# Kernel optimization log

Measured on AMD Instinct MI355X. Metric: run time of the kernel, lower is better.

## Reference

```python
import jax, jax.numpy as jnp
import numpy as np
from jax import lax

PH = PW = 7  # patch size


def _unfold2d(x, ph, pw):
    # x: [B, C, H, W] -> patches [B*Ho*Wo, C*ph*pw], channel-major like F.unfold
    B, C, H, W = x.shape
    patches = lax.conv_general_dilated_patches(
        x, filter_shape=(ph, pw), window_strides=(1, 1), padding='VALID')
    # patches: [B, C*ph*pw, Ho, Wo] with feature order (c, i, j) matching F.unfold
    Ho, Wo = H - ph + 1, W - pw + 1
    D = C * ph * pw
    q2d = patches.reshape(B, D, Ho * Wo).transpose(0, 2, 1).reshape(B * Ho * Wo, D)
    return q2d, (B, C, H, W, Ho, Wo, D)


def _fold2d_mean(res, shape_info):
    # res: [B*Ho*Wo, D] patch values -> overlap-add mean image [B, C, H, W]
    B, C, H, W, Ho, Wo, D = shape_info
    res = res.reshape(B, Ho, Wo, C, PH, PW)
    out = jnp.zeros((B, C, H, W), dtype=res.dtype)
    cnt = jnp.zeros((H, W), dtype=res.dtype)
    for di in range(PH):          # small fixed 7x7 loop over patch offsets
        for dj in range(PW):
            out = out.at[:, :, di:di + Ho, dj:dj + Wo].add(
                res[:, :, :, :, di, dj].transpose(0, 3, 1, 2))
            cnt = cnt.at[di:di + Ho, dj:dj + Wo].add(1.0)
    return out / cnt  # reduce='mean'


def setup_inputs() -> dict:
    key = jax.random.key(0)
    k1, k2, k3 = jax.random.split(key, 3)
    query = jax.random.normal(k1, (1, 3, 96, 96), dtype=jnp.float32)
    kmat = jax.random.normal(k2, (8100, 147), dtype=jnp.float32)
    vmat = jax.random.normal(k3, (8100, 147), dtype=jnp.float32)
    return {"query": query, "key": kmat, "value": vmat}


def reference(query, key, value):
    # 1) unfold query image into patch rows [Nq, D]
    q2d, shape_info = _unfold2d(query, PH, PW)
    # 2) nearest-neighbor lookup: squared-euclidean argmin over key rows
    qn = jnp.sum(q2d * q2d, axis=1, keepdims=True)        # [Nq, 1]
    kn = jnp.sum(key * key, axis=1)                       # [Nk]
    dist = qn + kn[None, :] - 2.0 * (q2d @ key.T)         # [Nq, Nk]
    idx = jnp.argmin(dist, axis=1)                        # [Nq]
    # 3) gather matched value patches and fold back (overlap-add mean)
    res = value[idx]                                      # [Nq, D]
    return _fold2d_mean(res, shape_info)
```

## Files before the change

### kernel.cpp

```cpp
#include <hip/hip_runtime.h>


#define NQ 8100
#define NK 8100
#define DD 147
#define HO 90
#define IMG 96
#define NCH 5
#define CST 262144
#define ARRN (NCH * CST)

typedef _Float16 half8 __attribute__((ext_vector_type(8)));
typedef float f32x4 __attribute__((ext_vector_type(4)));

__global__ void k_prep(const float* __restrict__ query, const float* __restrict__ key,
                       _Float16* __restrict__ Qh, _Float16* __restrict__ Ql,
                       _Float16* __restrict__ Kh, _Float16* __restrict__ Kl,
                       float* __restrict__ kn, unsigned long long* __restrict__ fidx64) {
    const int bx = blockIdx.x;
    const bool isK = (blockIdx.y != 0);

    if (bx >= 640) {
        if (!isK) return;
        int wave = threadIdx.x >> 6, lane = threadIdx.x & 63;
        int kb = ((bx - 640) * 4 + wave) * 16;
        for (int r = 0; r < 16; ++r) {
            int k = kb + r;
            float s = 0.f;
            if (k < NK)
                for (int d = lane; d < DD; d += 64) {
                    float v = key[k * DD + d];
                    s += v * v;
                }
#pragma unroll
            for (int off = 32; off; off >>= 1) s += __shfl_down(s, off, 64);
            if (lane == 0) {
                kn[k] = (k < NK) ? s : 1e30f;
                fidx64[k] = 0xFFFFFFFFFFFFFFFFull;
            }
        }
        return;
    }

    int t = bx * 256 + threadIdx.x;
    int c = t >> 15;
    int rem = t & 32767;
    int col = ((rem >> 6) << 4) + (rem & 15);
    int quad = (rem >> 4) & 3;
    int kbase = c * 32 + quad * 8;

    float v[8];
#pragma unroll
    for (int j = 0; j < 8; ++j) {
        int k = kbase + j;
        float x = 0.f;
        if (k < DD && col < NQ) {
            if (isK) {
                x = key[col * DD + k];
            } else {
                int c3 = k / 49, r2 = k - 49 * c3;
                int rr = r2 / 7, ss = r2 - 7 * rr;
                int y = col / HO, xx = col - HO * y;
                x = query[(c3 * IMG + y + rr) * IMG + xx + ss];
            }
        }
        v[j] = x;
    }
    half8 h8, l8;
#pragma unroll
    for (int j = 0; j < 8; ++j) {
        _Float16 h = (_Float16)v[j];
        h8[j] = h;
        l8[j] = (_Float16)(v[j] - (float)h);
    }
    if (isK) {
        *(half8*)(Kh + t * 8) = h8;
        *(half8*)(Kl + t * 8) = l8;
    } else {
        *(half8*)(Qh + t * 8) = h8;
        *(half8*)(Ql + t * 8) = l8;
    }
}

__launch_bounds__(256, 3)
__global__ void k_nn(const _Float16* __restrict__ Qh, const _Float16* __restrict__ Ql,
                     const _Float16* __restrict__ Kh, const _Float16* __restrict__ Kl,
                     const float* __restrict__ kn, unsigned long long* __restrict__ out) {
    __shared__ __align__(16) char smem[33792];

    const int tid = (int)threadIdx.x;
    const int wave = tid >> 6, lane = tid & 63;
    const int l15 = lane & 15, quad = lane >> 4;

    const int b = (int)blockIdx.x;
    const int xcd = b & 7;
    const int i = b >> 3;
    const int qt = (xcd >> 1) * 16 + (i & 15);
    const int kt = (xcd & 1) * 32 + (i >> 4);

    const int mbase = (wave >> 1) * 64;
    const int nbase = (wave & 1) * 64;
    const int q0 = qt * 128, n0 = kt * 128;

    const int agrp = (mbase >> 4);
    const int bgrp = (nbase >> 4);
    const _Float16* gQh = Qh + (qt * 8 + agrp) * 512 + lane * 8;
    const _Float16* gQl = Ql + (qt * 8 + agrp) * 512 + lane * 8;
    const _Float16* gKh = Kh + (kt * 8 + bgrp) * 512 + lane * 8;
    const _Float16* gKl = Kl + (kt * 8 + bgrp) * 512 + lane * 8;

    f32x4 acc[4][4];
#pragma unroll
    for (int ii = 0; ii < 4; ++ii)
#pragma unroll
        for (int j = 0; j < 4; ++j)
            acc[ii][j] = (f32x4)0.f;

#pragma unroll
    for (int c = 0; c < NCH; ++c) {
        half8 ah[4], al[4], bh[4], bl[4];
#pragma unroll
        for (int mt = 0; mt < 4; ++mt) {
            ah[mt] = *(const half8*)(gQh + c * CST + mt * 512);
            al[mt] = *(const half8*)(gQl + c * CST + mt * 512);
        }
#pragma unroll
        for (int nt = 0; nt < 4; ++nt) {
            bh[nt] = *(const half8*)(gKh + c * CST + nt * 512);
            bl[nt] = *(const half8*)(gKl + c * CST + nt * 512);
        }

        __builtin_amdgcn_s_setprio(1);
#pragma unroll
        for (int nt = 0; nt < 4; ++nt) {
#pragma unroll
            for (int mt = 0; mt < 4; ++mt) {
                acc[mt][nt] = __builtin_amdgcn_mfma_f32_16x16x32_f16(ah[mt], bh[nt], acc[mt][nt], 0, 0, 0);
                acc[mt][nt] = __builtin_amdgcn_mfma_f32_16x16x32_f16(ah[mt], bl[nt], acc[mt][nt], 0, 0, 0);
                acc[mt][nt] = __builtin_amdgcn_mfma_f32_16x16x32_f16(al[mt], bh[nt], acc[mt][nt], 0, 0, 0);
            }
        }
        __builtin_amdgcn_s_setprio(0);
    }

    float knv[4];
    int nglob[4];
#pragma unroll
    for (int nt = 0; nt < 4; ++nt) {
        nglob[nt] = n0 + nbase + nt * 16 + l15;
        knv[nt] = kn[nglob[nt]];
    }
    unsigned long long* redu = (unsigned long long*)smem;

#pragma unroll
    for (int mt = 0; mt < 4; ++mt)
#pragma unroll
        for (int r = 0; r < 4; ++r) {
            float bv = 1e38f;
            int bn = 0x7fffffff;
#pragma unroll
            for (int nt = 0; nt < 4; ++nt) {
                float d = knv[nt] - 2.0f * acc[mt][nt][r];
                if (d < bv) { bv = d; bn = nglob[nt]; }
            }
            int m = mbase + mt * 16 + quad * 4 + r;
            int cidx = (nbase >> 2) + l15;
            unsigned u = __float_as_uint(bv);
            u = (u & 0x80000000u) ? ~u : (u | 0x80000000u);
            redu[m * 33 + cidx] = ((unsigned long long)u << 32) | (unsigned)bn;
        }
    __syncthreads();

    {
        int row = tid >> 1;
        int base = (tid & 1) * 16;
        unsigned long long best = 0xFFFFFFFFFFFFFFFFull;
        const unsigned long long* rp = redu + row * 33 + base;
#pragma unroll
        for (int t2 = 0; t2 < 16; ++t2) {
            unsigned long long v = rp[t2];
            best = (v < best) ? v : best;
        }
        unsigned long long other = __shfl_xor(best, 1, 64);
        best = (other < best) ? other : best;
        if (!(tid & 1)) atomicMin(&out[q0 + row], best);
    }
}

__global__ void k_fold(const float* __restrict__ value,
                       const unsigned long long* __restrict__ fidx64,
                       float* __restrict__ out) {
    int t = blockIdx.x * 256 + threadIdx.x;
    int pix = t >> 3, s = t & 7;
    if (pix >= 3 * IMG * IMG) return;
    int c = pix / (IMG * IMG);
    int rem = pix % (IMG * IMG);
    int Y = rem / IMG, X = rem % IMG;

    float partial = 0.f;
    int yy = Y - s;
    if (s < 7 && (unsigned)yy < (unsigned)HO) {
        const unsigned* fidx32 = (const unsigned*)fidx64;
        const float* vbase = value + c * 49 + s * 7;
        int rows[7];
        bool oks[7];
#pragma unroll
        for (int j = 0; j < 7; ++j) {
            int xx = X - j;
            bool ok = (unsigned)xx < (unsigned)HO;
            int p = ok ? (yy * HO + xx) : 0;
            rows[j] = (int)fidx32[2 * p];
            oks[j] = ok;
        }
#pragma unroll
        for (int j = 0; j < 7; ++j) {
            float v = vbase[rows[j] * DD + j];
            if (oks[j]) partial += v;
        }
    }
    partial += __shfl_down(partial, 4, 8);
    partial += __shfl_down(partial, 2, 8);
    partial += __shfl_down(partial, 1, 8);
    if (s == 0) {
        int i0 = max(0, Y - (HO - 1)), i1 = min(6, Y);
        int j0 = max(0, X - (HO - 1)), j1 = min(6, X);
        float cnt = (float)((i1 - i0 + 1) * (j1 - j0 + 1));
        out[pix] = partial / cnt;
    }
}

extern "C" void kernel_launch(void* const* d_in, const int* in_sizes, int n_in,
                              void* d_out, int out_size, void* d_ws, size_t ws_size,
                              hipStream_t stream) {
    const float* query = (const float*)d_in[0];
    const float* key   = (const float*)d_in[1];
    const float* value = (const float*)d_in[2];
    float* out = (float*)d_out;

    _Float16* Qh = (_Float16*)d_ws;
    _Float16* Ql = Qh + ARRN;
    _Float16* Kh = Ql + ARRN;
    _Float16* Kl = Kh + ARRN;
    float* kn = (float*)(Kl + ARRN);
    unsigned long long* fidx64 = (unsigned long long*)(kn + 8192);

    dim3 gp(768, 2);
    k_prep<<<gp, 256, 0, stream>>>(query, key, Qh, Ql, Kh, Kl, kn, fidx64);
    k_nn<<<4096, 256, 0, stream>>>(Qh, Ql, Kh, Kl, kn, fidx64);
    k_fold<<<864, 256, 0, stream>>>(value, fidx64, out);
}
```

Before: 143.6 us.

## Switch NN distance GEMM to 32x32x16 MFMA with matching operand layout

Replaces the 16x16x32 f16 MFMA tiling with 32x32x16 MFMA instructions (2x2 tiles of 32x32 per wave) and rewrites the prep kernel's packed layout of the Q/K hi/lo halves to match the new operand fragment shape. The epilogue is adapted to the 32x32 accumulator register mapping and adds a lane-pair shuffle min before writing to shared memory, halving the shared writes. This aims to cut MFMA issue count and raise matrix throughput per instruction, but changes register usage and the reduction mapping.

```diff
diff --git a/kernel.cpp b/kernel.cpp
--- a/kernel.cpp
+++ b/kernel.cpp
@@ -11,7 +11,7 @@
 #define ARRN (NCH * CST)
 
 typedef _Float16 half8 __attribute__((ext_vector_type(8)));
-typedef float f32x4 __attribute__((ext_vector_type(4)));
+typedef float f32x16 __attribute__((ext_vector_type(16)));
 
 __global__ void k_prep(const float* __restrict__ query, const float* __restrict__ key,
                        _Float16* __restrict__ Qh, _Float16* __restrict__ Ql,
@@ -42,12 +42,13 @@
         return;
     }
 
-    int t = bx * 256 + threadIdx.x;
-    int c = t >> 15;
-    int rem = t & 32767;
-    int col = ((rem >> 6) << 4) + (rem & 15);
-    int quad = (rem >> 4) & 3;
-    int kbase = c * 32 + quad * 8;
+    int g8 = bx * 256 + threadIdx.x;
+    int lane = g8 & 63;
+    int s16 = (g8 >> 6) & 1;
+    int t32 = (g8 >> 7) & 255;
+    int c = g8 >> 15;
+    int col = t32 * 32 + (lane & 31);
+    int kbase = c * 32 + s16 * 16 + (lane >> 5) * 8;
 
     float v[8];
 #pragma unroll
@@ -74,11 +75,11 @@
         l8[j] = (_Float16)(v[j] - (float)h);
     }
     if (isK) {
-        *(half8*)(Kh + t * 8) = h8;
-        *(half8*)(Kl + t * 8) = l8;
+        *(half8*)(Kh + g8 * 8) = h8;
+        *(half8*)(Kl + g8 * 8) = l8;
     } else {
-        *(half8*)(Qh + t * 8) = h8;
-        *(half8*)(Ql + t * 8) = l8;
+        *(half8*)(Qh + g8 * 8) = h8;
+        *(half8*)(Ql + g8 * 8) = l8;
     }
 }
 
@@ -90,7 +91,7 @@
 
     const int tid = (int)threadIdx.x;
     const int wave = tid >> 6, lane = tid & 63;
-    const int l15 = lane & 15, quad = lane >> 4;
+    const int hi = lane >> 5;
 
     const int b = (int)blockIdx.x;
     const int xcd = b & 7;
@@ -102,72 +103,80 @@
     const int nbase = (wave & 1) * 64;
     const int q0 = qt * 128, n0 = kt * 128;
 
-    const int agrp = (mbase >> 4);
-    const int bgrp = (nbase >> 4);
-    const _Float16* gQh = Qh + (qt * 8 + agrp) * 512 + lane * 8;
-    const _Float16* gQl = Ql + (qt * 8 + agrp) * 512 + lane * 8;
-    const _Float16* gKh = Kh + (kt * 8 + bgrp) * 512 + lane * 8;
-    const _Float16* gKl = Kl + (kt * 8 + bgrp) * 512 + lane * 8;
-
-    f32x4 acc[4][4];
-#pragma unroll
-    for (int ii = 0; ii < 4; ++ii)
-#pragma unroll
-        for (int j = 0; j < 4; ++j)
-            acc[ii][j] = (f32x4)0.f;
+    const _Float16* gQh = Qh + ((qt * 4 + (wave >> 1) * 2) * 2) * 512 + lane * 8;
+    const _Float16* gQl = Ql + ((qt * 4 + (wave >> 1) * 2) * 2) * 512 + lane * 8;
+    const _Float16* gKh = Kh + ((kt * 4 + (wave & 1) * 2) * 2) * 512 + lane * 8;
+    const _Float16* gKl = Kl + ((kt * 4 + (wave & 1) * 2) * 2) * 512 + lane * 8;
+
+    f32x16 acc[2][2];
+#pragma unroll
+    for (int ii = 0; ii < 2; ++ii)
+#pragma unroll
+        for (int j = 0; j < 2; ++j)
+            acc[ii][j] = (f32x16)0.f;
 
 #pragma unroll
     for (int c = 0; c < NCH; ++c) {
-        half8 ah[4], al[4], bh[4], bl[4];
-#pragma unroll
-        for (int mt = 0; mt < 4; ++mt) {
-            ah[mt] = *(const half8*)(gQh + c * CST + mt * 512);
-            al[mt] = *(const half8*)(gQl + c * CST + mt * 512);
-        }
-#pragma unroll
-        for (int nt = 0; nt < 4; ++nt) {
-            bh[nt] = *(const half8*)(gKh + c * CST + nt * 512);
-            bl[nt] = *(const half8*)(gKl + c * CST + nt * 512);
-        }
+        half8 ah[2][2], al[2][2], bh[2][2], bl[2][2];
+#pragma unroll
+        for (int mt = 0; mt < 2; ++mt)
+#pragma unroll
+            for (int s = 0; s < 2; ++s) {
+                ah[mt][s] = *(const half8*)(gQh + c * CST + (mt * 2 + s) * 512);
+                al[mt][s] = *(const half8*)(gQl + c * CST + (mt * 2 + s) * 512);
+            }
+#pragma unroll
+        for (int nt = 0; nt < 2; ++nt)
+#pragma unroll
+            for (int s = 0; s < 2; ++s) {
+                bh[nt][s] = *(const half8*)(gKh + c * CST + (nt * 2 + s) * 512);
+                bl[nt][s] = *(const half8*)(gKl + c * CST + (nt * 2 + s) * 512);
+            }
 
         __builtin_amdgcn_s_setprio(1);
 #pragma unroll
-        for (int nt = 0; nt < 4; ++nt) {
-#pragma unroll
-            for (int mt = 0; mt < 4; ++mt) {
-                acc[mt][nt] = __builtin_amdgcn_mfma_f32_16x16x32_f16(ah[mt], bh[nt], acc[mt][nt], 0, 0, 0);
-                acc[mt][nt] = __builtin_amdgcn_mfma_f32_16x16x32_f16(ah[mt], bl[nt], acc[mt][nt], 0, 0, 0);
-                acc[mt][nt] = __builtin_amdgcn_mfma_f32_16x16x32_f16(al[mt], bh[nt], acc[mt][nt], 0, 0, 0);
-            }
-        }
+        for (int s = 0; s < 2; ++s)
+#pragma unroll
+            for (int nt = 0; nt < 2; ++nt)
+#pragma unroll
+                for (int mt = 0; mt < 2; ++mt) {
+                    acc[mt][nt] = __builtin_amdgcn_mfma_f32_32x32x16_f16(ah[mt][s], bh[nt][s], acc[mt][nt], 0, 0, 0);
+                    acc[mt][nt] = __builtin_amdgcn_mfma_f32_32x32x16_f16(ah[mt][s], bl[nt][s], acc[mt][nt], 0, 0, 0);
+                    acc[mt][nt] = __builtin_amdgcn_mfma_f32_32x32x16_f16(al[mt][s], bh[nt][s], acc[mt][nt], 0, 0, 0);
+                }
         __builtin_amdgcn_s_setprio(0);
     }
 
-    float knv[4];
-    int nglob[4];
-#pragma unroll
-    for (int nt = 0; nt < 4; ++nt) {
-        nglob[nt] = n0 + nbase + nt * 16 + l15;
+    float knv[2];
+    int nglob[2];
+#pragma unroll
+    for (int nt = 0; nt < 2; ++nt) {
+        nglob[nt] = n0 + nbase + nt * 32 + (lane & 31);
         knv[nt] = kn[nglob[nt]];
     }
     unsigned long long* redu = (unsigned long long*)smem;
-
-#pragma unroll
-    for (int mt = 0; mt < 4; ++mt)
-#pragma unroll
-        for (int r = 0; r < 4; ++r) {
+    const int cidx = (nbase >> 2) + ((lane & 31) >> 1);
+
+#pragma unroll
+    for (int mt = 0; mt < 2; ++mt)
+#pragma unroll
+        for (int reg = 0; reg < 16; ++reg) {
             float bv = 1e38f;
             int bn = 0x7fffffff;
 #pragma unroll
-            for (int nt = 0; nt < 4; ++nt) {
-                float d = knv[nt] - 2.0f * acc[mt][nt][r];
+            for (int nt = 0; nt < 2; ++nt) {
+                float d = knv[nt] - 2.0f * acc[mt][nt][reg];
                 if (d < bv) { bv = d; bn = nglob[nt]; }
             }
-            int m = mbase + mt * 16 + quad * 4 + r;
-            int cidx = (nbase >> 2) + l15;
             unsigned u = __float_as_uint(bv);
             u = (u & 0x80000000u) ? ~u : (u | 0x80000000u);
-            redu[m * 33 + cidx] = ((unsigned long long)u << 32) | (unsigned)bn;
+            unsigned long long pk = ((unsigned long long)u << 32) | (unsigned)bn;
+            unsigned long long po = __shfl_xor(pk, 1, 64);
+            pk = (po < pk) ? po : pk;
+            if (!(lane & 1)) {
+                int m = mbase + mt * 32 + (reg & 3) + 8 * (reg >> 2) + 4 * hi;
+                redu[m * 33 + cidx] = pk;
+            }
         }
     __syncthreads();
 
```

Result: slower. 157.4 us (+9.6%).

## Fuse prep, NN search and fold into one cooperative persistent kernel

Applied to the files above, without the earlier changes.

Replaces the three kernel launches with a single cooperative kernel of 512 persistent blocks. Grid-wide syncs separate the prep, nearest-neighbour and fold phases, and blocks loop over tiles and items. The aim is to remove launch gaps and tail effects between kernels. The per-row argmin reduction now pre-combines lane pairs with a shuffle, which halves shared memory and allows 2 blocks per CU. The risks are grid-sync overhead, lower occupancy from launch bounds of 2, and a static grid-stride assignment that may load-balance the NN tiles poorly.

```diff
diff --git a/kernel.cpp b/kernel.cpp
--- a/kernel.cpp
+++ b/kernel.cpp
@@ -1,4 +1,7 @@
 #include <hip/hip_runtime.h>
+#include <hip/hip_cooperative_groups.h>
+
+namespace cg = cooperative_groups;
 
 
 #define NQ 8100
@@ -9,9 +12,252 @@
 #define NCH 5
 #define CST 262144
 #define ARRN (NCH * CST)
+#define GRID 512
+#define GSIZE (GRID * 256)
 
 typedef _Float16 half8 __attribute__((ext_vector_type(8)));
 typedef float f32x4 __attribute__((ext_vector_type(4)));
+
+__device__ __forceinline__ void prep_item(int t, bool isK,
+                                          const float* __restrict__ query,
+                                          const float* __restrict__ key,
+                                          _Float16* __restrict__ Qh, _Float16* __restrict__ Ql,
+                                          _Float16* __restrict__ Kh, _Float16* __restrict__ Kl) {
+    int c = t >> 15;
+    int rem = t & 32767;
+    int col = ((rem >> 6) << 4) + (rem & 15);
+    int quad4 = (rem >> 4) & 3;
+    int kbase = c * 32 + quad4 * 8;
+
+    float v[8];
+#pragma unroll
+    for (int j = 0; j < 8; ++j) {
+        int k = kbase + j;
+        float x = 0.f;
+        if (k < DD && col < NQ) {
+            if (isK) {
+                x = key[col * DD + k];
+            } else {
+                int c3 = k / 49, r2 = k - 49 * c3;
+                int rr = r2 / 7, ss = r2 - 7 * rr;
+                int y = col / HO, xx = col - HO * y;
+                x = query[(c3 * IMG + y + rr) * IMG + xx + ss];
+            }
+        }
+        v[j] = x;
+    }
+    half8 h8, l8;
+#pragma unroll
+    for (int j = 0; j < 8; ++j) {
+        _Float16 h = (_Float16)v[j];
+        h8[j] = h;
+        l8[j] = (_Float16)(v[j] - (float)h);
+    }
+    if (isK) {
+        *(half8*)(Kh + t * 8) = h8;
+        *(half8*)(Kl + t * 8) = l8;
+    } else {
+        *(half8*)(Qh + t * 8) = h8;
+        *(half8*)(Ql + t * 8) = l8;
+    }
+}
+
+__device__ __forceinline__ void nn_tile(int b, int tid, char* smem,
+                                        const _Float16* __restrict__ Qh, const _Float16* __restrict__ Ql,
+                                        const _Float16* __restrict__ Kh, const _Float16* __restrict__ Kl,
+                                        const float* __restrict__ kn,
+                                        unsigned long long* __restrict__ fidx64) {
+    const int wave = tid >> 6, lane = tid & 63;
+    const int l15 = lane & 15, quad = lane >> 4;
+
+    const int xcd = b & 7;
+    const int i2 = b >> 3;
+    const int qt = (xcd >> 1) * 16 + (i2 & 15);
+    const int kt = (xcd & 1) * 32 + (i2 >> 4);
+    const int q0 = qt * 128, n0 = kt * 128;
+
+    const int mbase = (wave >> 1) * 64;
+    const int nbase = (wave & 1) * 64;
+    const int agrp = (mbase >> 4);
+    const int bgrp = (nbase >> 4);
+
+    const _Float16* gQh = Qh + (qt * 8 + agrp) * 512 + lane * 8;
+    const _Float16* gQl = Ql + (qt * 8 + agrp) * 512 + lane * 8;
+    const _Float16* gKh = Kh + (kt * 8 + bgrp) * 512 + lane * 8;
+    const _Float16* gKl = Kl + (kt * 8 + bgrp) * 512 + lane * 8;
+
+    f32x4 acc[4][4];
+#pragma unroll
+    for (int ii = 0; ii < 4; ++ii)
+#pragma unroll
+        for (int j = 0; j < 4; ++j)
+            acc[ii][j] = (f32x4)0.f;
+
+#pragma unroll
+    for (int c = 0; c < NCH; ++c) {
+        half8 ah[4], al[4], bh[4], bl[4];
+#pragma unroll
+        for (int mt = 0; mt < 4; ++mt) {
+            ah[mt] = *(const half8*)(gQh + c * CST + mt * 512);
+            al[mt] = *(const half8*)(gQl + c * CST + mt * 512);
+        }
+#pragma unroll
+        for (int nt = 0; nt < 4; ++nt) {
+            bh[nt] = *(const half8*)(gKh + c * CST + nt * 512);
+            bl[nt] = *(const half8*)(gKl + c * CST + nt * 512);
+        }
+
+        __builtin_amdgcn_s_setprio(1);
+#pragma unroll
+        for (int nt = 0; nt < 4; ++nt) {
+#pragma unroll
+            for (int mt = 0; mt < 4; ++mt) {
+                acc[mt][nt] = __builtin_amdgcn_mfma_f32_16x16x32_f16(ah[mt], bh[nt], acc[mt][nt], 0, 0, 0);
+                acc[mt][nt] = __builtin_amdgcn_mfma_f32_16x16x32_f16(ah[mt], bl[nt], acc[mt][nt], 0, 0, 0);
+                acc[mt][nt] = __builtin_amdgcn_mfma_f32_16x16x32_f16(al[mt], bh[nt], acc[mt][nt], 0, 0, 0);
+            }
+        }
+        __builtin_amdgcn_s_setprio(0);
+    }
+
+    float knv[4];
+    int nglob[4];
+#pragma unroll
+    for (int nt = 0; nt < 4; ++nt) {
+        nglob[nt] = n0 + nbase + nt * 16 + l15;
+        knv[nt] = kn[nglob[nt]];
+    }
+    unsigned long long* redu = (unsigned long long*)smem;
+    const int cidx2 = (nbase >> 3) + (l15 >> 1);
+
+#pragma unroll
+    for (int mt = 0; mt < 4; ++mt)
+#pragma unroll
+        for (int r = 0; r < 4; ++r) {
+            float bv = 1e38f;
+            int bn = 0x7fffffff;
+#pragma unroll
+            for (int nt = 0; nt < 4; ++nt) {
+                float d = knv[nt] - 2.0f * acc[mt][nt][r];
+                if (d < bv) { bv = d; bn = nglob[nt]; }
+            }
+            unsigned u = __float_as_uint(bv);
+            u = (u & 0x80000000u) ? ~u : (u | 0x80000000u);
+            unsigned long long pk = ((unsigned long long)u << 32) | (unsigned)bn;
+            unsigned long long po = __shfl_xor(pk, 1, 64);
+            pk = (po < pk) ? po : pk;
+            if (!(lane & 1)) {
+                int m = mbase + mt * 16 + quad * 4 + r;
+                redu[m * 17 + cidx2] = pk;
+            }
+        }
+    __syncthreads();
+
+    {
+        int row = tid >> 1;
+        int base = (tid & 1) * 8;
+        unsigned long long best = 0xFFFFFFFFFFFFFFFFull;
+        const unsigned long long* rp = redu + row * 17 + base;
+#pragma unroll
+        for (int t2 = 0; t2 < 8; ++t2) {
+            unsigned long long v = rp[t2];
+            best = (v < best) ? v : best;
+        }
+        unsigned long long other = __shfl_xor(best, 1, 64);
+        best = (other < best) ? other : best;
+        if (!(tid & 1)) atomicMin(&fidx64[q0 + row], best);
+    }
+    __syncthreads();
+}
+
+__device__ __forceinline__ void fold_item(int t, const float* __restrict__ value,
+                                          const unsigned long long* __restrict__ fidx64,
+                                          float* __restrict__ out) {
+    int pix = t >> 3, s = t & 7;
+    int c = pix / (IMG * IMG);
+    int rem = pix % (IMG * IMG);
+    int Y = rem / IMG, X = rem % IMG;
+
+    float partial = 0.f;
+    int yy = Y - s;
+    if (s < 7 && (unsigned)yy < (unsigned)HO) {
+        const unsigned* fidx32 = (const unsigned*)fidx64;
+        const float* vbase = value + c * 49 + s * 7;
+        int rows[7];
+        bool oks[7];
+#pragma unroll
+        for (int j = 0; j < 7; ++j) {
+            int xx = X - j;
+            bool ok = (unsigned)xx < (unsigned)HO;
+            int p = ok ? (yy * HO + xx) : 0;
+            rows[j] = (int)fidx32[2 * p];
+            oks[j] = ok;
+        }
+#pragma unroll
+        for (int j = 0; j < 7; ++j) {
+            float v = vbase[rows[j] * DD + j];
+            if (oks[j]) partial += v;
+        }
+    }
+    partial += __shfl_down(partial, 4, 8);
+    partial += __shfl_down(partial, 2, 8);
+    partial += __shfl_down(partial, 1, 8);
+    if (s == 0) {
+        int i0 = max(0, Y - (HO - 1)), i1 = min(6, Y);
+        int j0 = max(0, X - (HO - 1)), j1 = min(6, X);
+        float cnt = (float)((i1 - i0 + 1) * (j1 - j0 + 1));
+        out[pix] = partial / cnt;
+    }
+}
+
+__launch_bounds__(256, 2)
+__global__ void k_all(const float* __restrict__ query, const float* __restrict__ key,
+                      const float* __restrict__ value,
+                      _Float16* __restrict__ Qh, _Float16* __restrict__ Ql,
+                      _Float16* __restrict__ Kh, _Float16* __restrict__ Kl,
+                      float* __restrict__ kn, unsigned long long* __restrict__ fidx64,
+                      float* __restrict__ out) {
+    __shared__ __align__(16) char smem[17408];
+
+    const int tid = (int)threadIdx.x;
+    const int bid = (int)blockIdx.x;
+    const int gtid = bid * 256 + tid;
+    const int lane = tid & 63;
+
+    for (int item = gtid; item < 2 * (ARRN / 8); item += GSIZE) {
+        const bool isK = item >= (ARRN / 8);
+        prep_item(isK ? item - (ARRN / 8) : item, isK, query, key, Qh, Ql, Kh, Kl);
+    }
+    {
+        int wid = gtid >> 6;
+        int kb = wid * 4;
+        for (int r = 0; r < 4; ++r) {
+            int k = kb + r;
+            float s = 0.f;
+            if (k < NK)
+                for (int d = lane; d < DD; d += 64) {
+                    float v = key[k * DD + d];
+                    s += v * v;
+                }
+#pragma unroll
+            for (int off = 32; off; off >>= 1) s += __shfl_down(s, off, 64);
+            if (lane == 0) {
+                kn[k] = (k < NK) ? s : 1e30f;
+                fidx64[k] = 0xFFFFFFFFFFFFFFFFull;
+            }
+        }
+    }
+    __threadfence();
+    cg::this_grid().sync();
+
+    for (int b = bid; b < 4096; b += GRID)
+        nn_tile(b, tid, smem, Qh, Ql, Kh, Kl, kn, fidx64);
+    __threadfence();
+    cg::this_grid().sync();
+
+    for (int t = gtid; t < 3 * IMG * IMG * 8; t += GSIZE)
+        fold_item(t, value, fidx64, out);
+}
 
 __global__ void k_prep(const float* __restrict__ query, const float* __restrict__ key,
                        _Float16* __restrict__ Qh, _Float16* __restrict__ Ql,
@@ -19,7 +265,6 @@
                        float* __restrict__ kn, unsigned long long* __restrict__ fidx64) {
     const int bx = blockIdx.x;
     const bool isK = (blockIdx.y != 0);
-
     if (bx >= 640) {
         if (!isK) return;
         int wave = threadIdx.x >> 6, lane = threadIdx.x & 63;
@@ -41,192 +286,22 @@
         }
         return;
     }
-
-    int t = bx * 256 + threadIdx.x;
-    int c = t >> 15;
-    int rem = t & 32767;
-    int col = ((rem >> 6) << 4) + (rem & 15);
-    int quad = (rem >> 4) & 3;
-    int kbase = c * 32 + quad * 8;
-
-    float v[8];
-#pragma unroll
-    for (int j = 0; j < 8; ++j) {
-        int k = kbase + j;
-        float x = 0.f;
-        if (k < DD && col < NQ) {
-            if (isK) {
-                x = key[col * DD + k];
-            } else {
-                int c3 = k / 49, r2 = k - 49 * c3;
-                int rr = r2 / 7, ss = r2 - 7 * rr;
-                int y = col / HO, xx = col - HO * y;
-                x = query[(c3 * IMG + y + rr) * IMG + xx + ss];
-            }
-        }
-        v[j] = x;
-    }
-    half8 h8, l8;
-#pragma unroll
-    for (int j = 0; j < 8; ++j) {
-        _Float16 h = (_Float16)v[j];
-        h8[j] = h;
-        l8[j] = (_Float16)(v[j] - (float)h);
-    }
-    if (isK) {
-        *(half8*)(Kh + t * 8) = h8;
-        *(half8*)(Kl + t * 8) = l8;
-    } else {
-        *(half8*)(Qh + t * 8) = h8;
-        *(half8*)(Ql + t * 8) = l8;
-    }
+    prep_item(bx * 256 + threadIdx.x, isK, query, key, Qh, Ql, Kh, Kl);
 }
 
 __launch_bounds__(256, 3)
 __global__ void k_nn(const _Float16* __restrict__ Qh, const _Float16* __restrict__ Ql,
                      const _Float16* __restrict__ Kh, const _Float16* __restrict__ Kl,
                      const float* __restrict__ kn, unsigned long long* __restrict__ out) {
-    __shared__ __align__(16) char smem[33792];
-
-    const int tid = (int)threadIdx.x;
-    const int wave = tid >> 6, lane = tid & 63;
-    const int l15 = lane & 15, quad = lane >> 4;
-
-    const int b = (int)blockIdx.x;
-    const int xcd = b & 7;
-    const int i = b >> 3;
-    const int qt = (xcd >> 1) * 16 + (i & 15);
-    const int kt = (xcd & 1) * 32 + (i >> 4);
-
-    const int mbase = (wave >> 1) * 64;
-    const int nbase = (wave & 1) * 64;
-    const int q0 = qt * 128, n0 = kt * 128;
-
-    const int agrp = (mbase >> 4);
-    const int bgrp = (nbase >> 4);
-    const _Float16* gQh = Qh + (qt * 8 + agrp) * 512 + lane * 8;
-    const _Float16* gQl = Ql + (qt * 8 + agrp) * 512 + lane * 8;
-    const _Float16* gKh = Kh + (kt * 8 + bgrp) * 512 + lane * 8;
-    const _Float16* gKl = Kl + (kt * 8 + bgrp) * 512 + lane * 8;
-
-    f32x4 acc[4][4];
-#pragma unroll
-    for (int ii = 0; ii < 4; ++ii)
-#pragma unroll
-        for (int j = 0; j < 4; ++j)
-            acc[ii][j] = (f32x4)0.f;
-
-#pragma unroll
-    for (int c = 0; c < NCH; ++c) {
-        half8 ah[4], al[4], bh[4], bl[4];
-#pragma unroll
-        for (int mt = 0; mt < 4; ++mt) {
-            ah[mt] = *(const half8*)(gQh + c * CST + mt * 512);
-            al[mt] = *(const half8*)(gQl + c * CST + mt * 512);
-        }
-#pragma unroll
-        for (int nt = 0; nt < 4; ++nt) {
-            bh[nt] = *(const half8*)(gKh + c * CST + nt * 512);
-            bl[nt] = *(const half8*)(gKl + c * CST + nt * 512);
-        }
-
-        __builtin_amdgcn_s_setprio(1);
-#pragma unroll
-        for (int nt = 0; nt < 4; ++nt) {
-#pragma unroll
-            for (int mt = 0; mt < 4; ++mt) {
-                acc[mt][nt] = __builtin_amdgcn_mfma_f32_16x16x32_f16(ah[mt], bh[nt], acc[mt][nt], 0, 0, 0);
-                acc[mt][nt] = __builtin_amdgcn_mfma_f32_16x16x32_f16(ah[mt], bl[nt], acc[mt][nt], 0, 0, 0);
-                acc[mt][nt] = __builtin_amdgcn_mfma_f32_16x16x32_f16(al[mt], bh[nt], acc[mt][nt], 0, 0, 0);
-            }
-        }
-        __builtin_amdgcn_s_setprio(0);
-    }
-
-    float knv[4];
-    int nglob[4];
-#pragma unroll
-    for (int nt = 0; nt < 4; ++nt) {
-        nglob[nt] = n0 + nbase + nt * 16 + l15;
-        knv[nt] = kn[nglob[nt]];
-    }
-    unsigned long long* redu = (unsigned long long*)smem;
-
-#pragma unroll
-    for (int mt = 0; mt < 4; ++mt)
-#pragma unroll
-        for (int r = 0; r < 4; ++r) {
-            float bv = 1e38f;
-            int bn = 0x7fffffff;
-#pragma unroll
-            for (int nt = 0; nt < 4; ++nt) {
-                float d = knv[nt] - 2.0f * acc[mt][nt][r];
-                if (d < bv) { bv = d; bn = nglob[nt]; }
-            }
-            int m = mbase + mt * 16 + quad * 4 + r;
-            int cidx = (nbase >> 2) + l15;
-            unsigned u = __float_as_uint(bv);
-            u = (u & 0x80000000u) ? ~u : (u | 0x80000000u);
-            redu[m * 33 + cidx] = ((unsigned long long)u << 32) | (unsigned)bn;
-        }
-    __syncthreads();
-
-    {
-        int row = tid >> 1;
-        int base = (tid & 1) * 16;
-        unsigned long long best = 0xFFFFFFFFFFFFFFFFull;
-        const unsigned long long* rp = redu + row * 33 + base;
-#pragma unroll
-        for (int t2 = 0; t2 < 16; ++t2) {
-            unsigned long long v = rp[t2];
-            best = (v < best) ? v : best;
-        }
-        unsigned long long other = __shfl_xor(best, 1, 64);
-        best = (other < best) ? other : best;
-        if (!(tid & 1)) atomicMin(&out[q0 + row], best);
-    }
+    __shared__ __align__(16) char smem[17408];
+    nn_tile((int)blockIdx.x, (int)threadIdx.x, smem, Qh, Ql, Kh, Kl, kn, out);
 }
 
 __global__ void k_fold(const float* __restrict__ value,
                        const unsigned long long* __restrict__ fidx64,
                        float* __restrict__ out) {
     int t = blockIdx.x * 256 + threadIdx.x;
-    int pix = t >> 3, s = t & 7;
-    if (pix >= 3 * IMG * IMG) return;
-    int c = pix / (IMG * IMG);
-    int rem = pix % (IMG * IMG);
-    int Y = rem / IMG, X = rem % IMG;
-
-    float partial = 0.f;
-    int yy = Y - s;
-    if (s < 7 && (unsigned)yy < (unsigned)HO) {
-        const unsigned* fidx32 = (const unsigned*)fidx64;
-        const float* vbase = value + c * 49 + s * 7;
-        int rows[7];
-        bool oks[7];
-#pragma unroll
-        for (int j = 0; j < 7; ++j) {
-            int xx = X - j;
-            bool ok = (unsigned)xx < (unsigned)HO;
-            int p = ok ? (yy * HO + xx) : 0;
-            rows[j] = (int)fidx32[2 * p];
-            oks[j] = ok;
-        }
-#pragma unroll
-        for (int j = 0; j < 7; ++j) {
-            float v = vbase[rows[j] * DD + j];
-            if (oks[j]) partial += v;
-        }
-    }
-    partial += __shfl_down(partial, 4, 8);
-    partial += __shfl_down(partial, 2, 8);
-    partial += __shfl_down(partial, 1, 8);
-    if (s == 0) {
-        int i0 = max(0, Y - (HO - 1)), i1 = min(6, Y);
-        int j0 = max(0, X - (HO - 1)), j1 = min(6, X);
-        float cnt = (float)((i1 - i0 + 1) * (j1 - j0 + 1));
-        out[pix] = partial / cnt;
-    }
+    if (t < 3 * IMG * IMG * 8) fold_item(t, value, fidx64, out);
 }
 
 extern "C" void kernel_launch(void* const* d_in, const int* in_sizes, int n_in,
@@ -244,8 +319,16 @@
     float* kn = (float*)(Kl + ARRN);
     unsigned long long* fidx64 = (unsigned long long*)(kn + 8192);
 
-    dim3 gp(768, 2);
-    k_prep<<<gp, 256, 0, stream>>>(query, key, Qh, Ql, Kh, Kl, kn, fidx64);
-    k_nn<<<4096, 256, 0, stream>>>(Qh, Ql, Kh, Kl, kn, fidx64);
-    k_fold<<<864, 256, 0, stream>>>(value, fidx64, out);
-}
+    void* args[] = {(void*)&query, (void*)&key, (void*)&value,
+                    (void*)&Qh, (void*)&Ql, (void*)&Kh, (void*)&Kl,
+                    (void*)&kn, (void*)&fidx64, (void*)&out};
+    hipError_t e = hipLaunchCooperativeKernel((const void*)k_all, dim3(GRID), dim3(256),
+                                              args, 0, stream);
+    if (e != hipSuccess) {
+        (void)hipGetLastError();
+        dim3 gp(768, 2);
+        k_prep<<<gp, 256, 0, stream>>>(query, key, Qh, Ql, Kh, Kl, kn, fidx64);
+        k_nn<<<4096, 256, 0, stream>>>(Qh, Ql, Kh, Kl, kn, fidx64);
+        k_fold<<<864, 256, 0, stream>>>(value, fidx64, out);
+    }
+}
```

Result: slower. 308.8 us (+115.0%).
